# Performance work log

Hardware: AMD Instinct MI355X
Metric: run time of the kernel (lower is better)

The kernel has to match this reference:

```python
import jax, jax.numpy as jnp
import numpy as np

B = 4096          # players (batch)
DEG = 64          # asteroids per player
A = B * DEG       # total asteroids
E = A             # one edge per asteroid (asteroid -> its player)
PD, AD, ED = 5, 3, 7
HID = 64
HEADS = 4
OUT = HID         # GATv2Conv out_channels (concat=False -> mean over heads)
L = 2             # num_layers
NEG_SLOPE = 0.2
LN_EPS = 1e-5


def setup_inputs() -> dict:
    key = jax.random.key(0)
    ks = jax.random.split(key, 20)
    f = jnp.float32
    inp = {}
    inp["player_feat"] = jax.random.normal(ks[0], (B, PD), f)
    inp["asteroid_feat"] = jax.random.normal(ks[1], (A, AD), f)
    src = jnp.arange(E, dtype=jnp.int32)
    dst = src // DEG                      # player batch index per edge
    inp["edge_index"] = jnp.stack([src, dst])  # [2, E] int32
    inp["edge_attr"] = jax.random.normal(ks[2], (E, ED), f)
    sc = 0.1
    # input projections
    inp["Wp"] = jax.random.normal(ks[3], (PD, HID), f) * sc
    inp["bp"] = jnp.zeros((HID,), f)
    inp["Wa"] = jax.random.normal(ks[4], (AD, HID), f) * sc
    inp["ba"] = jnp.zeros((HID,), f)
    # per-layer GATv2 params (stacked over L)
    inp["Wl"] = jax.random.normal(ks[5], (L, HID, HEADS * OUT), f) * sc
    inp["bl"] = jnp.zeros((L, HEADS * OUT), f)
    inp["Wr"] = jax.random.normal(ks[6], (L, HID, HEADS * OUT), f) * sc
    inp["br"] = jnp.zeros((L, HEADS * OUT), f)
    inp["We"] = jax.random.normal(ks[7], (L, ED, HEADS * OUT), f) * sc
    inp["att"] = jax.random.normal(ks[8], (L, HEADS, OUT), f) * sc
    inp["bias"] = jnp.zeros((L, OUT), f)
    inp["ln_g"] = jnp.ones((L, HID), f)
    inp["ln_b"] = jnp.zeros((L, HID), f)
    return inp


def _layer_norm(x, g, b):
    mu = jnp.mean(x, axis=-1, keepdims=True)
    var = jnp.mean(jnp.square(x - mu), axis=-1, keepdims=True)
    return (x - mu) * jax.lax.rsqrt(var + LN_EPS) * g + b


def _gatv2(x, src, dst, edge_attr, Wl, bl, Wr, br, We, att, bias, n_nodes):
    # x: [N, HID]; src/dst: [E]; PyG GATv2Conv, add_self_loops=False, concat=False
    xl = (x @ Wl + bl).reshape(-1, HEADS, OUT)   # source transform
    xr = (x @ Wr + br).reshape(-1, HEADS, OUT)   # target transform
    ea = (edge_attr @ We).reshape(-1, HEADS, OUT)
    e = xl[src] + xr[dst] + ea                   # [E, H, O]
    e = jnp.where(e >= 0, e, NEG_SLOPE * e)      # LeakyReLU(0.2)
    logits = jnp.einsum('eho,ho->eh', e, att)    # [E, H]
    # segment softmax over incoming edges of each target node
    m = jax.ops.segment_max(logits, dst, num_segments=n_nodes)
    al = jnp.exp(logits - m[dst])
    den = jax.ops.segment_sum(al, dst, num_segments=n_nodes)
    alpha = al / den[dst]                        # [E, H]
    msg = alpha[:, :, None] * xl[src]            # [E, H, O]
    out = jax.ops.segment_sum(msg, dst, num_segments=n_nodes)  # [N, H, O]
    return jnp.mean(out, axis=1) + bias          # concat=False -> head mean


def reference(player_feat, asteroid_feat, edge_index, edge_attr,
              Wp, bp, Wa, ba, Wl, bl, Wr, br, We, att, bias, ln_g, ln_b):
    batch = player_feat.shape[0]
    h_p = jax.nn.relu(player_feat @ Wp + bp)
    h_a = jax.nn.relu(asteroid_feat @ Wa + ba)
    x = jnp.concatenate([h_p, h_a], axis=0)      # [N, HID]
    n_nodes = x.shape[0]
    src = edge_index[0] + batch                  # asteroid local -> global idx
    dst = edge_index[1]
    for i in range(L):
        x_new = _gatv2(x, src, dst, edge_attr, Wl[i], bl[i], Wr[i], br[i],
                       We[i], att[i], bias[i], n_nodes)
        x = _layer_norm(x + jax.nn.relu(x_new), ln_g[i], ln_b[i])
    return x[:batch]
```

## Files before the change

kernel.cpp:

```cpp
#include <hip/hip_runtime.h>


typedef __bf16 bf16x8 __attribute__((ext_vector_type(8)));
typedef float  f32x4  __attribute__((ext_vector_type(4)));

union FragU { unsigned short u[8]; bf16x8 v; };

__device__ __forceinline__ float bf2f(unsigned short u) {
    union { unsigned int i; float f; } v; v.i = ((unsigned int)u) << 16; return v.f;
}
__device__ __forceinline__ unsigned short f2bf(float f) {
    union { __bf16 b; unsigned short u; } x; x.b = (__bf16)f; return x.u;
}

#define NEG_SLOPE 0.2f
#define LN_EPS 1e-5f
#define XS 88

struct Smem {
    __align__(16) unsigned short xa[64 * XS];
    __align__(16) unsigned short xpb[64];
    float outp[256];
    float xp[64];
    float afs[192];
    float rbs[64], gs[64], bs[64];
};

#define WS_NEED (163840 + 3 * 8192)

__global__ __launch_bounds__(256) void prep_weights(
    const float* __restrict__ Wl, const float* __restrict__ Wr,
    const float* __restrict__ We, const float* __restrict__ bl,
    const float* __restrict__ att, const float* __restrict__ br,
    unsigned short* __restrict__ wlf, unsigned short* __restrict__ wrf,
    unsigned short* __restrict__ wef, f32x4* __restrict__ blq,
    f32x4* __restrict__ attq, f32x4* __restrict__ brq)
{
    int i = blockIdx.x * 256 + threadIdx.x;
    int jj = i & 7, t = (i >> 3) & 255, frag = (i >> 11) & 7, layer = (i >> 14) & 1;
    int nt = frag >> 1, ko = frag & 1;
    int c = (t >> 6) * 64 + nt * 16 + (t & 15);
    int kb = ko * 32 + ((t >> 4) & 3) * 8;
    wlf[i] = f2bf(Wl[layer * 16384 + (kb + jj) * 256 + c]);
    wrf[i] = f2bf(Wr[layer * 16384 + (kb + jj) * 256 + c]);
    if (i < 16384) {
        int j2 = i & 7, t2 = (i >> 3) & 255, n2 = (i >> 11) & 3, l2 = (i >> 13) & 1;
        int q2 = (t2 >> 4) & 3;
        int c2 = (t2 >> 6) * 64 + n2 * 16 + (t2 & 15);
        wef[i] = (q2 == 0 && j2 < 7) ? f2bf(We[l2 * 1792 + j2 * 256 + c2])
                                     : (unsigned short)0;
    }
    if (i < 512) {
        int lyr = i >> 8, tt = i & 255;
        int hb = (tt >> 6) * 64, mm = tt & 15;
        f32x4 b, a, r;
        #pragma unroll
        for (int n = 0; n < 4; ++n) {
            int cc = hb + n * 16 + mm;
            b[n] = bl[lyr * 256 + cc];
            a[n] = att[lyr * 256 + cc];
            r[n] = br[lyr * 256 + cc];
        }
        blq[i] = b; attq[i] = a; brq[i] = r;
    }
}

template <bool WS>
__global__ __launch_bounds__(256) void gnn_main(
    const float* __restrict__ pf, const float* __restrict__ af,
    const float* __restrict__ eat, const float* __restrict__ Wp,
    const float* __restrict__ bp, const float* __restrict__ Wa,
    const float* __restrict__ ba, const float* __restrict__ Wl,
    const float* __restrict__ bl, const float* __restrict__ Wr,
    const float* __restrict__ br, const float* __restrict__ We,
    const float* __restrict__ att, const float* __restrict__ bias,
    const float* __restrict__ lng, const float* __restrict__ lnb,
    const unsigned short* __restrict__ wlf, const unsigned short* __restrict__ wrf,
    const unsigned short* __restrict__ wef, const f32x4* __restrict__ blq,
    const f32x4* __restrict__ attq, const f32x4* __restrict__ brq,
    float* __restrict__ out)
{
    __shared__ Smem sm;
    const int p = blockIdx.x, t = threadIdx.x;
    const int w = t >> 6, l = t & 63, q = l >> 4, m = l & 15;
    const int cbase = w * 64;

    if (t < 192) sm.afs[t] = af[p * 192 + t];
    if (t < 64) {
        sm.rbs[t] = fmaxf(bias[t], 0.f);
        sm.gs[t] = lng[t];
        sm.bs[t] = lnb[t];
        float acc = bp[t];
        #pragma unroll
        for (int d = 0; d < 5; ++d) acc += pf[p * 5 + d] * Wp[d * 64 + t];
        float xp0 = fmaxf(acc, 0.f);
        sm.xp[t] = xp0;
        sm.xpb[t] = f2bf(xp0);
    }
    __syncthreads();
    {
        const int k = t & 63;
        float wa0 = Wa[k], wa1 = Wa[64 + k], wa2 = Wa[128 + k], bak = ba[k];
        #pragma unroll
        for (int rep = 0; rep < 16; ++rep) {
            int j = rep * 4 + (t >> 6);
            float acc = bak + sm.afs[j * 3] * wa0 + sm.afs[j * 3 + 1] * wa1
                      + sm.afs[j * 3 + 2] * wa2;
            sm.xa[j * XS + k] = f2bf(fmaxf(acc, 0.f));
        }
    }
    #pragma unroll
    for (int idx = t; idx < 512; idx += 256) {
        int j = idx >> 3, d = idx & 7;
        sm.xa[j * XS + 64 + d] = (d < 7) ? f2bf(eat[(p * 64 + j) * 7 + d])
                                         : (unsigned short)0;
    }
    __syncthreads();

    f32x4 accT[16];

    for (int layer = 0; layer < 2; ++layer) {
        f32x4 blv, atv, brv;
        if constexpr (WS) {
            blv = blq[layer * 256 + t];
            atv = attq[layer * 256 + t];
            brv = brq[layer * 256 + t];
        } else {
            #pragma unroll
            for (int nt = 0; nt < 4; ++nt) {
                int c = cbase + nt * 16 + m;
                blv[nt] = bl[layer * 256 + c];
                atv[nt] = att[layer * 256 + c];
                brv[nt] = br[layer * 256 + c];
            }
        }

        float xrc[4];
        {
            FragU xf0, xf1;
            xf0.v = *reinterpret_cast<const bf16x8*>(&sm.xpb[q * 8]);
            xf1.v = *reinterpret_cast<const bf16x8*>(&sm.xpb[32 + q * 8]);
            #pragma unroll
            for (int nt = 0; nt < 4; ++nt) {
                FragU r0, r1;
                if constexpr (WS) {
                    r0.v = *reinterpret_cast<const bf16x8*>(&wrf[((layer * 8 + nt * 2 + 0) * 256 + t) * 8]);
                    r1.v = *reinterpret_cast<const bf16x8*>(&wrf[((layer * 8 + nt * 2 + 1) * 256 + t) * 8]);
                } else {
                    int c = cbase + nt * 16 + m;
                    #pragma unroll
                    for (int jj = 0; jj < 8; ++jj) {
                        r0.u[jj] = f2bf(Wr[layer * 16384 + (q * 8 + jj) * 256 + c]);
                        r1.u[jj] = f2bf(Wr[layer * 16384 + (32 + q * 8 + jj) * 256 + c]);
                    }
                }
                f32x4 cx = { brv[nt], brv[nt], brv[nt], brv[nt] };
                cx = __builtin_amdgcn_mfma_f32_16x16x32_bf16(xf0.v, r0.v, cx, 0, 0, 0);
                cx = __builtin_amdgcn_mfma_f32_16x16x32_bf16(xf1.v, r1.v, cx, 0, 0, 0);
                xrc[nt] = cx[0];
            }
        }

        FragU bfr[8];
        bf16x8 ebf[4];
        if constexpr (WS) {
            #pragma unroll
            for (int f = 0; f < 8; ++f)
                bfr[f].v = *reinterpret_cast<const bf16x8*>(&wlf[((layer * 8 + f) * 256 + t) * 8]);
            #pragma unroll
            for (int nt = 0; nt < 4; ++nt)
                ebf[nt] = *reinterpret_cast<const bf16x8*>(&wef[((layer * 4 + nt) * 256 + t) * 8]);
        } else {
            const float* Wli = Wl + layer * 16384;
            #pragma unroll
            for (int nt = 0; nt < 4; ++nt) {
                int c = cbase + nt * 16 + m;
                #pragma unroll
                for (int ko = 0; ko < 2; ++ko) {
                    int kb = ko * 32 + q * 8;
                    #pragma unroll
                    for (int jj = 0; jj < 8; ++jj)
                        bfr[nt * 2 + ko].u[jj] = f2bf(Wli[(kb + jj) * 256 + c]);
                }
                FragU e;
                #pragma unroll
                for (int jj = 0; jj < 8; ++jj)
                    e.u[jj] = (q == 0 && jj < 7) ? f2bf(We[layer * 1792 + jj * 256 + c])
                                                 : (unsigned short)0;
                ebf[nt] = e.v;
            }
        }

        float lp[16];
        #pragma unroll
        for (int i = 0; i < 16; ++i) lp[i] = 0.f;

        #pragma unroll
        for (int mt = 0; mt < 4; ++mt) {
            const int row = mt * 16 + m;
            bf16x8 a0 = *reinterpret_cast<const bf16x8*>(&sm.xa[row * XS + q * 8]);
            bf16x8 a1 = *reinterpret_cast<const bf16x8*>(&sm.xa[row * XS + 32 + q * 8]);
            bf16x8 a2 = *reinterpret_cast<const bf16x8*>(&sm.xa[row * XS + 64]);
            #pragma unroll
            for (int nt = 0; nt < 4; ++nt) {
                f32x4 c1 = { blv[nt], blv[nt], blv[nt], blv[nt] };
                c1 = __builtin_amdgcn_mfma_f32_16x16x32_bf16(a0, bfr[nt * 2 + 0].v, c1, 0, 0, 0);
                c1 = __builtin_amdgcn_mfma_f32_16x16x32_bf16(a1, bfr[nt * 2 + 1].v, c1, 0, 0, 0);
                accT[mt * 4 + nt] = c1;
                f32x4 c2 = { xrc[nt], xrc[nt], xrc[nt], xrc[nt] };
                c2 = __builtin_amdgcn_mfma_f32_16x16x32_bf16(a2, ebf[nt], c2, 0, 0, 0);
                #pragma unroll
                for (int r = 0; r < 4; ++r) {
                    float ev = c1[r] + c2[r];
                    ev = fmaxf(ev, NEG_SLOPE * ev);
                    lp[mt * 4 + r] += ev * atv[nt];
                }
            }
        }

        #pragma unroll
        for (int i = 0; i < 16; ++i) {
            float v = lp[i];
            v += __shfl_xor(v, 1, 64);
            v += __shfl_xor(v, 2, 64);
            v += __shfl_xor(v, 4, 64);
            v += __shfl_xor(v, 8, 64);
            lp[i] = v;
        }
        float mx = lp[0];
        #pragma unroll
        for (int i = 1; i < 16; ++i) mx = fmaxf(mx, lp[i]);
        mx = fmaxf(mx, __shfl_xor(mx, 16, 64));
        mx = fmaxf(mx, __shfl_xor(mx, 32, 64));
        float den = 0.f;
        #pragma unroll
        for (int i = 0; i < 16; ++i) { lp[i] = __expf(lp[i] - mx); den += lp[i]; }
        den += __shfl_xor(den, 16, 64);
        den += __shfl_xor(den, 32, 64);
        const float rden = 1.f / den;

        #pragma unroll
        for (int nt = 0; nt < 4; ++nt) {
            float s = 0.f;
            #pragma unroll
            for (int i = 0; i < 16; ++i) s += lp[i] * accT[(i >> 2) * 4 + nt][i & 3];
            s *= rden;
            s += __shfl_xor(s, 16, 64);
            s += __shfl_xor(s, 32, 64);
            if (q == 0) sm.outp[cbase + nt * 16 + m] = s;
        }
        __syncthreads();

        if (layer == 0) {
            {
                const int j = t >> 2, part = t & 3;
                unsigned short* rowp = &sm.xa[j * XS + part * 16];
                FragU A0, A1;
                A0.v = *reinterpret_cast<const bf16x8*>(rowp);
                A1.v = *reinterpret_cast<const bf16x8*>(rowp + 8);
                float v[16], sum = 0.f, sq = 0.f;
                #pragma unroll
                for (int i = 0; i < 16; ++i) {
                    unsigned short us = (i < 8) ? A0.u[i] : A1.u[i - 8];
                    float x = bf2f(us) + sm.rbs[part * 16 + i];
                    v[i] = x; sum += x; sq += x * x;
                }
                sum += __shfl_xor(sum, 1, 64); sq += __shfl_xor(sq, 1, 64);
                sum += __shfl_xor(sum, 2, 64); sq += __shfl_xor(sq, 2, 64);
                float mu = sum * (1.f / 64.f);
                float var = sq * (1.f / 64.f) - mu * mu;
                float rs = rsqrtf(var + LN_EPS);
                FragU O0, O1;
                #pragma unroll
                for (int i = 0; i < 16; ++i) {
                    int col = part * 16 + i;
                    unsigned short ub = f2bf((v[i] - mu) * rs * sm.gs[col] + sm.bs[col]);
                    if (i < 8) O0.u[i] = ub; else O1.u[i - 8] = ub;
                }
                *reinterpret_cast<bf16x8*>(rowp) = O0.v;
                *reinterpret_cast<bf16x8*>(rowp + 8) = O1.v;
            }
            if (t < 64) {
                float xnew = 0.25f * (sm.outp[t] + sm.outp[64 + t] + sm.outp[128 + t] + sm.outp[192 + t])
                           + bias[t];
                float v = sm.xp[t] + fmaxf(xnew, 0.f);
                float sum = v, sq = v * v;
                #pragma unroll
                for (int msk = 1; msk <= 32; msk <<= 1) {
                    sum += __shfl_xor(sum, msk, 64);
                    sq  += __shfl_xor(sq,  msk, 64);
                }
                float mu = sum * (1.f / 64.f);
                float var = sq * (1.f / 64.f) - mu * mu;
                float y = (v - mu) * rsqrtf(var + LN_EPS) * lng[t] + lnb[t];
                sm.xp[t] = y;
                sm.xpb[t] = f2bf(y);
            }
            __syncthreads();
        } else {
            if (t < 64) {
                float xnew = 0.25f * (sm.outp[t] + sm.outp[64 + t] + sm.outp[128 + t] + sm.outp[192 + t])
                           + bias[64 + t];
                float v = sm.xp[t] + fmaxf(xnew, 0.f);
                float sum = v, sq = v * v;
                #pragma unroll
                for (int msk = 1; msk <= 32; msk <<= 1) {
                    sum += __shfl_xor(sum, msk, 64);
                    sq  += __shfl_xor(sq,  msk, 64);
                }
                float mu = sum * (1.f / 64.f);
                float var = sq * (1.f / 64.f) - mu * mu;
                float y = (v - mu) * rsqrtf(var + LN_EPS) * lng[64 + t] + lnb[64 + t];
                out[p * 64 + t] = y;
            }
        }
    }
}

extern "C" void kernel_launch(void* const* d_in, const int* in_sizes, int n_in,
                              void* d_out, int out_size, void* d_ws, size_t ws_size,
                              hipStream_t stream) {
    const float* pf   = (const float*)d_in[0];
    const float* af   = (const float*)d_in[1];
    const float* eat  = (const float*)d_in[3];
    const float* Wp   = (const float*)d_in[4];
    const float* bp   = (const float*)d_in[5];
    const float* Wa   = (const float*)d_in[6];
    const float* ba   = (const float*)d_in[7];
    const float* Wl   = (const float*)d_in[8];
    const float* bl   = (const float*)d_in[9];
    const float* Wr   = (const float*)d_in[10];
    const float* br   = (const float*)d_in[11];
    const float* We   = (const float*)d_in[12];
    const float* att  = (const float*)d_in[13];
    const float* bias = (const float*)d_in[14];
    const float* lng  = (const float*)d_in[15];
    const float* lnb  = (const float*)d_in[16];
    float* out = (float*)d_out;

    const int B = in_sizes[0] / 5;
    unsigned short* wlf = (unsigned short*)d_ws;
    unsigned short* wrf = wlf + 32768;
    unsigned short* wef = wrf + 32768;
    f32x4* blq  = (f32x4*)((char*)d_ws + 163840);
    f32x4* attq = blq + 512;
    f32x4* brq  = attq + 512;

    if (ws_size >= WS_NEED) {
        prep_weights<<<dim3(128), dim3(256), 0, stream>>>(
            Wl, Wr, We, bl, att, br, wlf, wrf, wef, blq, attq, brq);
        gnn_main<true><<<dim3(B), dim3(256), 0, stream>>>(
            pf, af, eat, Wp, bp, Wa, ba, Wl, bl, Wr, br, We, att, bias, lng, lnb,
            wlf, wrf, wef, blq, attq, brq, out);
    } else {
        gnn_main<false><<<dim3(B), dim3(256), 0, stream>>>(
            pf, af, eat, Wp, bp, Wa, ba, Wl, bl, Wr, br, We, att, bias, lng, lnb,
            wlf, wrf, wef, blq, attq, brq, out);
    }
}
```

Baseline: 187.4 us.

## Aggregate attention-weighted inputs before projection instead of keeping per-edge xl tiles

Uses linearity: the weighted sum of projected source features equals the projection of the attention-weighted sum of raw source features. Each head first computes z = sum_j alpha_j * x_j from shared memory, then applies one small MFMA projection. This frees the 16 accT accumulator registers, folds xr and bias into the MFMA init, and allows a tighter launch bound (5 blocks). It adds an LDS round trip for the logits, extra barriers, and bf16 rounding of z, which introduces a small precision difference.

```diff
diff --git a/kernel.cpp b/kernel.cpp
--- a/kernel.cpp
+++ b/kernel.cpp
@@ -20,6 +20,8 @@
 struct Smem {
     __align__(16) unsigned short xa[64 * XS];
     __align__(16) unsigned short xpb[64];
+    __align__(16) unsigned short zb[256];
+    __align__(16) float lpb4[4 * 64 * 4];
     float outp[256];
     float xp[64];
     float afs[192];
@@ -66,7 +68,7 @@
 }
 
 template <bool WS>
-__global__ __launch_bounds__(256) void gnn_main(
+__global__ __launch_bounds__(256, 5) void gnn_main(
     const float* __restrict__ pf, const float* __restrict__ af,
     const float* __restrict__ eat, const float* __restrict__ Wp,
     const float* __restrict__ bp, const float* __restrict__ Wa,
@@ -117,8 +119,6 @@
     }
     __syncthreads();
 
-    f32x4 accT[16];
-
     for (int layer = 0; layer < 2; ++layer) {
         f32x4 blv, atv, brv;
         if constexpr (WS) {
@@ -203,16 +203,14 @@
             bf16x8 a2 = *reinterpret_cast<const bf16x8*>(&sm.xa[row * XS + 64]);
             #pragma unroll
             for (int nt = 0; nt < 4; ++nt) {
-                f32x4 c1 = { blv[nt], blv[nt], blv[nt], blv[nt] };
-                c1 = __builtin_amdgcn_mfma_f32_16x16x32_bf16(a0, bfr[nt * 2 + 0].v, c1, 0, 0, 0);
-                c1 = __builtin_amdgcn_mfma_f32_16x16x32_bf16(a1, bfr[nt * 2 + 1].v, c1, 0, 0, 0);
-                accT[mt * 4 + nt] = c1;
-                f32x4 c2 = { xrc[nt], xrc[nt], xrc[nt], xrc[nt] };
-                c2 = __builtin_amdgcn_mfma_f32_16x16x32_bf16(a2, ebf[nt], c2, 0, 0, 0);
+                float sd = blv[nt] + xrc[nt];
+                f32x4 c = { sd, sd, sd, sd };
+                c = __builtin_amdgcn_mfma_f32_16x16x32_bf16(a0, bfr[nt * 2 + 0].v, c, 0, 0, 0);
+                c = __builtin_amdgcn_mfma_f32_16x16x32_bf16(a1, bfr[nt * 2 + 1].v, c, 0, 0, 0);
+                c = __builtin_amdgcn_mfma_f32_16x16x32_bf16(a2, ebf[nt], c, 0, 0, 0);
                 #pragma unroll
                 for (int r = 0; r < 4; ++r) {
-                    float ev = c1[r] + c2[r];
-                    ev = fmaxf(ev, NEG_SLOPE * ev);
+                    float ev = fmaxf(c[r], NEG_SLOPE * c[r]);
                     lp[mt * 4 + r] += ev * atv[nt];
                 }
             }
@@ -223,31 +221,61 @@
             float v = lp[i];
             v += __shfl_xor(v, 1, 64);
             v += __shfl_xor(v, 2, 64);
-            v += __shfl_xor(v, 4, 64);
-            v += __shfl_xor(v, 8, 64);
             lp[i] = v;
         }
-        float mx = lp[0];
-        #pragma unroll
-        for (int i = 1; i < 16; ++i) mx = fmaxf(mx, lp[i]);
-        mx = fmaxf(mx, __shfl_xor(mx, 16, 64));
-        mx = fmaxf(mx, __shfl_xor(mx, 32, 64));
-        float den = 0.f;
-        #pragma unroll
-        for (int i = 0; i < 16; ++i) { lp[i] = __expf(lp[i] - mx); den += lp[i]; }
-        den += __shfl_xor(den, 16, 64);
-        den += __shfl_xor(den, 32, 64);
-        const float rden = 1.f / den;
-
-        #pragma unroll
-        for (int nt = 0; nt < 4; ++nt) {
-            float s = 0.f;
-            #pragma unroll
-            for (int i = 0; i < 16; ++i) s += lp[i] * accT[(i >> 2) * 4 + nt][i & 3];
-            s *= rden;
-            s += __shfl_xor(s, 16, 64);
-            s += __shfl_xor(s, 32, 64);
-            if (q == 0) sm.outp[cbase + nt * 16 + m] = s;
+        if ((m & 3) == 0) {
+            #pragma unroll
+            for (int i = 0; i < 16; ++i) {
+                int j = (i >> 2) * 16 + q * 4 + (i & 3);
+                sm.lpb4[(w * 64 + j) * 4 + (m >> 2)] = lp[i];
+            }
+        }
+        __syncthreads();
+
+        float al;
+        {
+            f32x4 pr = *reinterpret_cast<const f32x4*>(&sm.lpb4[(w * 64 + l) * 4]);
+            float lg = (pr[0] + pr[1]) + (pr[2] + pr[3]);
+            float mx = lg;
+            #pragma unroll
+            for (int msk = 1; msk <= 32; msk <<= 1) mx = fmaxf(mx, __shfl_xor(mx, msk, 64));
+            al = __expf(lg - mx);
+            float den = al;
+            #pragma unroll
+            for (int msk = 1; msk <= 32; msk <<= 1) den += __shfl_xor(den, msk, 64);
+            al /= den;
+        }
+
+        {
+            float z0 = 0.f, z1 = 0.f, z2 = 0.f, z3 = 0.f;
+            #pragma unroll
+            for (int j = 0; j < 64; j += 4) {
+                float s0 = __shfl(al, j, 64);
+                float s1 = __shfl(al, j + 1, 64);
+                float s2 = __shfl(al, j + 2, 64);
+                float s3 = __shfl(al, j + 3, 64);
+                z0 += s0 * bf2f(sm.xa[j * XS + l]);
+                z1 += s1 * bf2f(sm.xa[(j + 1) * XS + l]);
+                z2 += s2 * bf2f(sm.xa[(j + 2) * XS + l]);
+                z3 += s3 * bf2f(sm.xa[(j + 3) * XS + l]);
+            }
+            sm.zb[w * 64 + l] = f2bf((z0 + z1) + (z2 + z3));
+        }
+        __syncthreads();
+
+        {
+            bf16x8 zf0 = *reinterpret_cast<const bf16x8*>(&sm.zb[w * 64 + q * 8]);
+            bf16x8 zf1 = *reinterpret_cast<const bf16x8*>(&sm.zb[w * 64 + 32 + q * 8]);
+            float oc[4];
+            #pragma unroll
+            for (int nt = 0; nt < 4; ++nt) {
+                f32x4 c = { blv[nt], blv[nt], blv[nt], blv[nt] };
+                c = __builtin_amdgcn_mfma_f32_16x16x32_bf16(zf0, bfr[nt * 2 + 0].v, c, 0, 0, 0);
+                c = __builtin_amdgcn_mfma_f32_16x16x32_bf16(zf1, bfr[nt * 2 + 1].v, c, 0, 0, 0);
+                oc[nt] = c[0];
+            }
+            float osel = (q == 0) ? oc[0] : (q == 1) ? oc[1] : (q == 2) ? oc[2] : oc[3];
+            sm.outp[t] = osel;
         }
         __syncthreads();
 
```

Result: slower. 300.7 us (+60.4%).
